# Optimization experiments

Measured on AMD Instinct MI355X. Metric: run time of the kernel, lower is better.

Reference implementation:

```python
import jax, jax.numpy as jnp
import numpy as np

B, N, T, E, R, NSEL = 128, 1000, 50, 32000, 4, 500
F0, CF = 3, 20
FS = 2 * CF + F0  # 43


def _conv(x, w, b):
    # NCHW valid conv, stride 1
    y = jax.lax.conv_general_dilated(x, w, (1, 1), 'VALID',
                                     dimension_numbers=('NCHW', 'OIHW', 'NCHW'))
    return y + b[None, :, None, None]


def setup_inputs() -> dict:
    key = jax.random.key(0)
    ks = jax.random.split(key, 20)
    s = 0.1
    return {
        'observation': jax.random.normal(ks[0], (B, F0, N, T), jnp.float32),
        'last_action': jax.random.uniform(ks[1], (B, NSEL + 1), jnp.float32),
        'w_s1': jax.random.normal(ks[2], (3, 3, 1, 3), jnp.float32) * s,
        'b_s1': jax.random.normal(ks[3], (3,), jnp.float32) * s,
        'w_s2': jax.random.normal(ks[4], (20, 3, 1, 48), jnp.float32) * s,
        'b_s2': jax.random.normal(ks[5], (20,), jnp.float32) * s,
        'w_m1': jax.random.normal(ks[6], (3, 3, 1, 21), jnp.float32) * s,
        'b_m1': jax.random.normal(ks[7], (3,), jnp.float32) * s,
        'w_m2': jax.random.normal(ks[8], (20, 3, 1, 30), jnp.float32) * s,
        'b_m2': jax.random.normal(ks[9], (20,), jnp.float32) * s,
        'w_rel': jax.random.normal(ks[10], (R, FS, FS), jnp.float32) * s,
        'w_root': jax.random.normal(ks[11], (FS, FS), jnp.float32) * s,
        'b_g': jax.random.normal(ks[12], (FS,), jnp.float32) * s,
        'w_fin': jax.random.normal(ks[13], (1, 2 * FS + 1, 1, 1), jnp.float32) * s,
        'b_fin': jax.random.normal(ks[14], (1,), jnp.float32) * s,
        'edge_index': jax.random.randint(ks[15], (2, E), 0, N, jnp.int64) if jax.config.jax_enable_x64 else jax.random.randint(ks[15], (2, E), 0, N).astype(jnp.int32),
        'edge_type': jax.random.randint(ks[16], (E,), 0, R).astype(jnp.int32),
        'nodes_to_select': jnp.sort(jax.random.randint(ks[17], (NSEL,), 0, N)).astype(jnp.int32),
    }


def reference(observation, last_action, w_s1, b_s1, w_s2, b_s2, w_m1, b_m1,
              w_m2, b_m2, w_rel, w_root, b_g, w_fin, b_fin,
              edge_index, edge_type, nodes_to_select):
    # temporal feature extraction
    short = jax.nn.relu(_conv(jax.nn.relu(_conv(observation, w_s1, b_s1)), w_s2, b_s2))
    mid = jax.nn.relu(_conv(jax.nn.relu(_conv(observation, w_m1, b_m1)), w_m2, b_m2))
    long = jax.nn.relu(jnp.max(observation, axis=3, keepdims=True))
    temporal = jnp.concatenate([short, mid, long], axis=1)  # [B, 43, N, 1]

    x = temporal[:, :, :, 0].transpose(0, 2, 1)  # [B, N, F]

    # RGCNConv with per-relation mean aggregation
    src, dst = edge_index[0], edge_index[1]
    xw = jnp.einsum('bnf,rfg->bnrg', x, w_rel)        # [B, N, R, F]
    msgs = xw[:, src, edge_type, :]                   # [B, E, F] gather
    seg = dst * R + edge_type                         # per (node, relation) segment
    agg = jax.vmap(lambda m: jax.ops.segment_sum(m, seg, num_segments=N * R))(msgs)
    cnt = jax.ops.segment_sum(jnp.ones((E,), x.dtype), seg, num_segments=N * R)
    inv = jnp.where(cnt > 0, 1.0 / cnt, 0.0)
    agg = (agg * inv[None, :, None]).reshape(B, N, R, FS).sum(axis=2)
    gout = jax.nn.leaky_relu(agg + x @ w_root + b_g, 0.01)  # [B, N, F]

    graph_features = gout.transpose(0, 2, 1)[..., None]     # [B, F, N, 1]
    feat = jnp.concatenate([temporal, graph_features], axis=1)  # [B, 86, N, 1]
    feat = feat[:, :, nodes_to_select, :]                       # [B, 86, NSEL, 1]
    last_stocks = last_action[:, 1:].reshape(B, 1, NSEL, 1)
    feat = jnp.concatenate([last_stocks, feat], axis=1)         # [B, 87, NSEL, 1]

    o = jnp.einsum('bcn,oc->bon', feat[..., 0], w_fin[:, :, 0, 0]) + b_fin[None, :, None]
    o = jnp.concatenate([jnp.zeros((B, 1, 1), o.dtype), o], axis=2)[:, 0, :]  # [B, NSEL+1]
    return jax.nn.softmax(o / 1.0, axis=-1)
```

## Files before the change

kernel.cpp:

```cpp
#include <hip/hip_runtime.h>
#include <math.h>

#define Bn 128
#define Nn 1000
#define Tn 50
#define En 32000
#define Rn 4
#define FSn 43
#define NSELn 500
#define NFtot (Nn * FSn)

__global__ __launch_bounds__(256, 4) void k_temporal(
    const float* __restrict__ obs,
    const float* __restrict__ w_s1, const float* __restrict__ b_s1,
    const float* __restrict__ w_s2, const float* __restrict__ b_s2,
    const float* __restrict__ w_m1, const float* __restrict__ b_m1,
    const float* __restrict__ w_m2, const float* __restrict__ b_m2,
    float* __restrict__ x)
{
    __shared__ float lds[3 * 64 * 51];

    const int b     = blockIdx.x;
    const int tile0 = blockIdx.y * 64;
    const int tid   = threadIdx.x;
    const int lane  = tid & 63;
    const int w     = __builtin_amdgcn_readfirstlane(tid >> 6);
    const int nrows = (Nn - tile0) < 64 ? (Nn - tile0) : 64;

    for (int c = 0; c < 3; ++c) {
        const float* srcp = obs + ((size_t)(b * 3 + c) * Nn + tile0) * Tn;
        for (int idx = tid; idx < nrows * Tn; idx += 256) {
            const int r = idx / Tn;
            const int t = idx - r * Tn;
            lds[(c * 64 + r) * 51 + t] = srcp[idx];
        }
    }
    __syncthreads();

    const int rb0 = (0 * 64 + lane) * 51;
    const int rb1 = (1 * 64 + lane) * 51;
    const int rb2 = (2 * 64 + lane) * 51;

    float acc[20];
    float mx0 = -1e30f, mx1 = -1e30f, mx2 = -1e30f;

    if (w < 2) {
        #pragma unroll
        for (int o = 0; o < 20; ++o) acc[o] = (w == 0) ? b_s2[o] : 0.f;

        const float s10 = b_s1[0], s11 = b_s1[1], s12 = b_s1[2];
        const int t0 = w * 24;

        #pragma unroll 1
        for (int t = t0; t < t0 + 24; ++t) {
            float v0 = s10, v1 = s11, v2 = s12;
            #pragma unroll
            for (int c = 0; c < 3; ++c) {
                const int base = (c * 64 + lane) * 51 + t;
                const float o0 = lds[base + 0];
                const float o1 = lds[base + 1];
                const float o2 = lds[base + 2];
                v0 += o0 * w_s1[(0 * 3 + c) * 3 + 0] + o1 * w_s1[(0 * 3 + c) * 3 + 1] + o2 * w_s1[(0 * 3 + c) * 3 + 2];
                v1 += o0 * w_s1[(1 * 3 + c) * 3 + 0] + o1 * w_s1[(1 * 3 + c) * 3 + 1] + o2 * w_s1[(1 * 3 + c) * 3 + 2];
                v2 += o0 * w_s1[(2 * 3 + c) * 3 + 0] + o1 * w_s1[(2 * 3 + c) * 3 + 1] + o2 * w_s1[(2 * 3 + c) * 3 + 2];
            }
            v0 = fmaxf(v0, 0.f); v1 = fmaxf(v1, 0.f); v2 = fmaxf(v2, 0.f);
            #pragma unroll
            for (int o = 0; o < 20; ++o) {
                acc[o] += v0 * w_s2[(o * 3 + 0) * 48 + t]
                        + v1 * w_s2[(o * 3 + 1) * 48 + t]
                        + v2 * w_s2[(o * 3 + 2) * 48 + t];
            }
        }

        const int l0 = w * 25;
        #pragma unroll 1
        for (int t = l0; t < l0 + 25; ++t) {
            mx0 = fmaxf(mx0, lds[rb0 + t]);
            mx1 = fmaxf(mx1, lds[rb1 + t]);
            mx2 = fmaxf(mx2, lds[rb2 + t]);
        }
    } else {
        #pragma unroll
        for (int o = 0; o < 20; ++o) acc[o] = (w == 2) ? b_m2[o] : 0.f;

        const float m10 = b_m1[0], m11 = b_m1[1], m12 = b_m1[2];
        const int t0 = (w - 2) * 15;

        #pragma unroll 1
        for (int t = t0; t < t0 + 15; ++t) {
            float u0 = m10, u1 = m11, u2 = m12;
            #pragma unroll
            for (int c = 0; c < 3; ++c) {
                const int base = (c * 64 + lane) * 51 + t;
                #pragma unroll
                for (int d = 0; d < 21; ++d) {
                    const float ov = lds[base + d];
                    u0 += ov * w_m1[(0 * 3 + c) * 21 + d];
                    u1 += ov * w_m1[(1 * 3 + c) * 21 + d];
                    u2 += ov * w_m1[(2 * 3 + c) * 21 + d];
                }
            }
            u0 = fmaxf(u0, 0.f); u1 = fmaxf(u1, 0.f); u2 = fmaxf(u2, 0.f);
            #pragma unroll
            for (int o = 0; o < 20; ++o) {
                acc[o] += u0 * w_m2[(o * 3 + 0) * 30 + t]
                        + u1 * w_m2[(o * 3 + 1) * 30 + t]
                        + u2 * w_m2[(o * 3 + 2) * 30 + t];
            }
        }
    }

    __syncthreads();
    float* pshort = lds;
    float* plong  = lds + 20 * 64;
    float* pmid   = lds + 23 * 64;

    if (w == 1) {
        #pragma unroll
        for (int o = 0; o < 20; ++o) pshort[o * 64 + lane] = acc[o];
        plong[0 * 64 + lane] = mx0;
        plong[1 * 64 + lane] = mx1;
        plong[2 * 64 + lane] = mx2;
    }
    if (w == 3) {
        #pragma unroll
        for (int o = 0; o < 20; ++o) pmid[o * 64 + lane] = acc[o];
    }
    __syncthreads();

    if (lane < nrows) {
        float* xp = x + ((size_t)b * Nn + tile0 + lane) * FSn;
        if (w == 0) {
            #pragma unroll
            for (int o = 0; o < 20; ++o)
                xp[o] = fmaxf(acc[o] + pshort[o * 64 + lane], 0.f);
            xp[40] = fmaxf(fmaxf(mx0, plong[0 * 64 + lane]), 0.f);
            xp[41] = fmaxf(fmaxf(mx1, plong[1 * 64 + lane]), 0.f);
            xp[42] = fmaxf(fmaxf(mx2, plong[2 * 64 + lane]), 0.f);
        } else if (w == 2) {
            #pragma unroll
            for (int o = 0; o < 20; ++o)
                xp[20 + o] = fmaxf(acc[o] + pmid[o * 64 + lane], 0.f);
        }
    }
}

__global__ __launch_bounds__(256) void k_transpose(const float* __restrict__ x,
                                                   float* __restrict__ xT)
{
    __shared__ float tile[64][129];
    const int c0  = blockIdx.x * 64;
    const int tid = threadIdx.x;

    const int j  = tid & 63;
    const int bs = tid >> 6;
    for (int bb = bs; bb < Bn; bb += 4) {
        int c = c0 + j;
        if (c < NFtot) tile[j][bb] = x[(size_t)bb * NFtot + c];
    }
    __syncthreads();

    const int b  = tid & 127;
    for (int jj = (tid >> 7); jj < 64; jj += 2) {
        int c = c0 + jj;
        if (c < NFtot) xT[(size_t)c * Bn + b] = tile[jj][b];
    }
}

__global__ void k_zero(int* __restrict__ cnt, int* __restrict__ pos)
{
    int i = blockIdx.x * blockDim.x + threadIdx.x;
    if (i < 4096) { cnt[i] = 0; pos[i] = 0; }
}

__global__ void k_count(const int* __restrict__ ei, const int* __restrict__ et,
                        int* __restrict__ cnt)
{
    int e = blockIdx.x * blockDim.x + threadIdx.x;
    if (e < En) {
        int dst = ei[En + e];
        atomicAdd(&cnt[dst * Rn + et[e]], 1);
    }
}

__global__ __launch_bounds__(1024) void k_scan(const int* __restrict__ cnt,
                                               int* __restrict__ off)
{
    __shared__ int sums[1024];
    int tid = threadIdx.x;
    int base = tid * 4;
    int c[4];
    int ts = 0;
    #pragma unroll
    for (int k = 0; k < 4; ++k) {
        int i = base + k;
        c[k] = (i < Nn * Rn) ? cnt[i] : 0;
        ts += c[k];
    }
    sums[tid] = ts;
    __syncthreads();
    for (int d = 1; d < 1024; d <<= 1) {
        int t = 0;
        if (tid >= d) t = sums[tid - d];
        __syncthreads();
        sums[tid] += t;
        __syncthreads();
    }
    int excl = sums[tid] - ts;
    #pragma unroll
    for (int k = 0; k < 4; ++k) {
        int i = base + k;
        off[i] = excl;
        excl += c[k];
    }
}

__global__ void k_fill(const int* __restrict__ ei, const int* __restrict__ et,
                       const int* __restrict__ off, int* __restrict__ pos,
                       int* __restrict__ csr)
{
    int e = blockIdx.x * blockDim.x + threadIdx.x;
    if (e < En) {
        int src = ei[e];
        int dst = ei[En + e];
        int seg = dst * Rn + et[e];
        int p = atomicAdd(&pos[seg], 1);
        csr[off[seg] + p] = src;
    }
}

__global__ __launch_bounds__(512) void k_gather(
    const float* __restrict__ xT,
    const float* __restrict__ w_rel, const float* __restrict__ w_root,
    const float* __restrict__ b_g,
    const float* __restrict__ w_fin, const float* __restrict__ b_fin,
    const float* __restrict__ la,
    const int* __restrict__ csr, const int* __restrict__ off,
    const int* __restrict__ cnt, const int* __restrict__ sel,
    float* __restrict__ logitT)
{
    __shared__ int   srcs[Rn][128];
    __shared__ int   scnt[Rn];
    __shared__ int   tcnt[Rn];
    __shared__ float red[FSn + 1][Bn];

    const int i   = blockIdx.x;
    const int dst = sel[i];
    const int tid = threadIdx.x;
    const int fs  = tid >> 7;
    const int b   = tid & 127;

    {
        const int r = fs;
        const int j = b;
        const int c = cnt[dst * Rn + r];
        const int o = off[dst * Rn + r];
        if (j == 0) { tcnt[r] = c; scnt[r] = (c < 128) ? c : 128; }
        if (j < c && j < 128) srcs[r][j] = csr[o + j];
    }
    __syncthreads();

    const int f0 = fs * 11;
    const int nf = (fs == 3) ? 10 : 11;

    float a[5][11];
    #pragma unroll
    for (int rr = 0; rr < 5; ++rr)
        #pragma unroll
        for (int k = 0; k < 11; ++k) a[rr][k] = 0.f;

    #pragma unroll
    for (int r = 0; r < Rn; ++r) {
        const int c = scnt[r];
        for (int j = 0; j < c; ++j) {
            const int src = srcs[r][j];
            const float* xp = xT + ((size_t)src * FSn + f0) * Bn + b;
            #pragma unroll
            for (int k = 0; k < 11; ++k)
                if (k < nf) a[r][k] += xp[(size_t)k * Bn];
        }
    }
    {
        const float* xp = xT + ((size_t)dst * FSn + f0) * Bn + b;
        #pragma unroll
        for (int k = 0; k < 11; ++k)
            if (k < nf) a[4][k] += xp[(size_t)k * Bn];
    }
    #pragma unroll
    for (int r = 0; r < Rn; ++r) {
        const int c = tcnt[r];
        const float iv = (c > 0) ? 1.f / (float)c : 0.f;
        #pragma unroll
        for (int k = 0; k < 11; ++k) a[r][k] *= iv;
    }

    float accg[FSn];
    #pragma unroll
    for (int g = 0; g < FSn; ++g) accg[g] = 0.f;
    float psum = 0.f;

    #pragma unroll
    for (int k = 0; k < 11; ++k) {
        if (k < nf) {
            const int f = f0 + k;
            #pragma unroll
            for (int rr = 0; rr < 5; ++rr) {
                const float av = a[rr][k];
                const float* wrow = (rr < 4)
                    ? (w_rel + ((size_t)rr * FSn + f) * FSn)
                    : (w_root + (size_t)f * FSn);
                #pragma unroll
                for (int g = 0; g < FSn; ++g) accg[g] += av * wrow[g];
            }
            psum += a[4][k] * w_fin[1 + f];
        }
    }

    if (fs == 3) {
        #pragma unroll
        for (int g = 0; g < FSn; ++g) red[g][b] = accg[g];
        red[FSn][b] = psum;
    }
    __syncthreads();
    if (fs == 2) {
        #pragma unroll
        for (int g = 0; g < FSn; ++g) red[g][b] += accg[g];
        red[FSn][b] += psum;
    }
    __syncthreads();
    if (fs == 1) {
        #pragma unroll
        for (int g = 0; g < FSn; ++g) red[g][b] += accg[g];
        red[FSn][b] += psum;
    }
    __syncthreads();
    if (fs == 0) {
        float logit = b_fin[0] + w_fin[0] * la[(size_t)b * (NSELn + 1) + 1 + i]
                    + psum + red[FSn][b];
        #pragma unroll
        for (int g = 0; g < FSn; ++g) {
            float v = accg[g] + red[g][b] + b_g[g];
            v = (v > 0.f) ? v : 0.01f * v;
            logit += v * w_fin[44 + g];
        }
        logitT[(size_t)i * Bn + b] = logit;
    }
}

__global__ __launch_bounds__(512) void k_softmax(const float* __restrict__ logitT,
                                                 float* __restrict__ out)
{
    __shared__ float red[512];
    const int b   = blockIdx.x;
    const int tid = threadIdx.x;

    const float l = (tid < NSELn) ? logitT[(size_t)tid * Bn + b] : -1e30f;
    red[tid] = l;
    __syncthreads();
    for (int s = 256; s > 0; s >>= 1) {
        if (tid < s) red[tid] = fmaxf(red[tid], red[tid + s]);
        __syncthreads();
    }
    const float m = fmaxf(red[0], 0.f);
    __syncthreads();

    const float e = (tid < NSELn) ? expf(l - m) : 0.f;
    red[tid] = e;
    __syncthreads();
    for (int s = 256; s > 0; s >>= 1) {
        if (tid < s) red[tid] += red[tid + s];
        __syncthreads();
    }
    const float e0  = expf(-m);
    const float inv = 1.f / (red[0] + e0);

    if (tid == 0) out[(size_t)b * (NSELn + 1)] = e0 * inv;
    if (tid < NSELn) out[(size_t)b * (NSELn + 1) + 1 + tid] = e * inv;
}

extern "C" void kernel_launch(void* const* d_in, const int* in_sizes, int n_in,
                              void* d_out, int out_size, void* d_ws, size_t ws_size,
                              hipStream_t stream)
{
    const float* obs    = (const float*)d_in[0];
    const float* la     = (const float*)d_in[1];
    const float* w_s1   = (const float*)d_in[2];
    const float* b_s1   = (const float*)d_in[3];
    const float* w_s2   = (const float*)d_in[4];
    const float* b_s2   = (const float*)d_in[5];
    const float* w_m1   = (const float*)d_in[6];
    const float* b_m1   = (const float*)d_in[7];
    const float* w_m2   = (const float*)d_in[8];
    const float* b_m2   = (const float*)d_in[9];
    const float* w_rel  = (const float*)d_in[10];
    const float* w_root = (const float*)d_in[11];
    const float* b_g    = (const float*)d_in[12];
    const float* w_fin  = (const float*)d_in[13];
    const float* b_fin  = (const float*)d_in[14];
    const int*   ei     = (const int*)d_in[15];
    const int*   et     = (const int*)d_in[16];
    const int*   sel    = (const int*)d_in[17];
    float*       out    = (float*)d_out;

    float* x      = (float*)d_ws;
    float* xT     = x + 5504000;
    int*   cnt    = (int*)(xT + 5504000);
    int*   offb   = cnt + 4096;
    int*   pos    = offb + 4096;
    int*   csr    = pos + 4096;
    float* logitT = x;

    hipLaunchKernelGGL(k_zero,  dim3(16),  dim3(256), 0, stream, cnt, pos);
    hipLaunchKernelGGL(k_count, dim3((En + 255) / 256), dim3(256), 0, stream, ei, et, cnt);
    hipLaunchKernelGGL(k_scan,  dim3(1),   dim3(1024), 0, stream, cnt, offb);
    hipLaunchKernelGGL(k_fill,  dim3((En + 255) / 256), dim3(256), 0, stream, ei, et, offb, pos, csr);

    hipLaunchKernelGGL(k_temporal, dim3(Bn, (Nn + 63) / 64), dim3(256), 0, stream,
                       obs, w_s1, b_s1, w_s2, b_s2, w_m1, b_m1, w_m2, b_m2, x);

    hipLaunchKernelGGL(k_transpose, dim3((NFtot + 63) / 64), dim3(256), 0, stream, x, xT);

    hipLaunchKernelGGL(k_gather, dim3(NSELn), dim3(512), 0, stream,
                       xT, w_rel, w_root, b_g, w_fin, b_fin, la,
                       csr, offb, cnt, sel, logitT);

    hipLaunchKernelGGL(k_softmax, dim3(Bn), dim3(512), 0, stream, logitT, out);
}
```

Measured before the change: 258.4 us.

## Split graph gather into per-relation aggregation kernel and restructure temporal convolutions

The fused gather-plus-transform kernel is split in two. A new kernel runs one block per (selected node, relation) and does a float4 vectorised neighbour sum into a workspace buffer. A second kernel reads these means and applies the relation and root weights. This gives four times more blocks for the memory-bound gather, at the cost of an extra global round trip. The temporal kernel is also changed: the short conv gets a sliding-window register reuse, and the mid conv is rewritten as a fully unrolled scatter over input positions so each LDS value is read once instead of 21 times. This raises register pressure, and the workspace layout is reorganised so the larger abar buffer fits.

```diff
diff --git a/kernel.cpp b/kernel.cpp
--- a/kernel.cpp
+++ b/kernel.cpp
@@ -10,6 +10,48 @@
 #define NSELn 500
 #define NFtot (Nn * FSn)
 
+template<int T0>
+__device__ __forceinline__ void mid_part(const float* __restrict__ lds, int lane,
+    const float* __restrict__ w_m1, const float* __restrict__ w_m2,
+    float bm0, float bm1v, float bm2, float* __restrict__ acc)
+{
+    float y0[15], y1[15], y2[15];
+    #pragma unroll
+    for (int t = 0; t < 15; ++t) { y0[t] = bm0; y1[t] = bm1v; y2[t] = bm2; }
+
+    const int rb0 = (0 * 64 + lane) * 51;
+    const int rb1 = (1 * 64 + lane) * 51;
+    const int rb2 = (2 * 64 + lane) * 51;
+
+    #pragma unroll
+    for (int tau = T0; tau < T0 + 35; ++tau) {
+        const int tlo = (tau - 20 > T0) ? (tau - 20) : T0;
+        const int thi = (tau < T0 + 14) ? tau : (T0 + 14);
+        const float o0 = lds[rb0 + tau];
+        const float o1 = lds[rb1 + tau];
+        const float o2 = lds[rb2 + tau];
+        #pragma unroll
+        for (int t = tlo; t <= thi; ++t) {
+            const int d = tau - t;
+            y0[t - T0] += o0 * w_m1[  0 + d] + o1 * w_m1[ 21 + d] + o2 * w_m1[ 42 + d];
+            y1[t - T0] += o0 * w_m1[ 63 + d] + o1 * w_m1[ 84 + d] + o2 * w_m1[105 + d];
+            y2[t - T0] += o0 * w_m1[126 + d] + o1 * w_m1[147 + d] + o2 * w_m1[168 + d];
+        }
+    }
+    #pragma unroll
+    for (int tt = 0; tt < 15; ++tt) {
+        const float u0 = fmaxf(y0[tt], 0.f);
+        const float u1 = fmaxf(y1[tt], 0.f);
+        const float u2 = fmaxf(y2[tt], 0.f);
+        #pragma unroll
+        for (int o = 0; o < 20; ++o) {
+            acc[o] += u0 * w_m2[(o * 3 + 0) * 30 + T0 + tt]
+                    + u1 * w_m2[(o * 3 + 1) * 30 + T0 + tt]
+                    + u2 * w_m2[(o * 3 + 2) * 30 + T0 + tt];
+        }
+    }
+}
+
 __global__ __launch_bounds__(256, 4) void k_temporal(
     const float* __restrict__ obs,
     const float* __restrict__ w_s1, const float* __restrict__ b_s1,
@@ -37,10 +79,6 @@
     }
     __syncthreads();
 
-    const int rb0 = (0 * 64 + lane) * 51;
-    const int rb1 = (1 * 64 + lane) * 51;
-    const int rb2 = (2 * 64 + lane) * 51;
-
     float acc[20];
     float mx0 = -1e30f, mx1 = -1e30f, mx2 = -1e30f;
 
@@ -50,31 +88,44 @@
 
         const float s10 = b_s1[0], s11 = b_s1[1], s12 = b_s1[2];
         const int t0 = w * 24;
-
-        #pragma unroll 1
-        for (int t = t0; t < t0 + 24; ++t) {
-            float v0 = s10, v1 = s11, v2 = s12;
-            #pragma unroll
-            for (int c = 0; c < 3; ++c) {
-                const int base = (c * 64 + lane) * 51 + t;
-                const float o0 = lds[base + 0];
-                const float o1 = lds[base + 1];
-                const float o2 = lds[base + 2];
-                v0 += o0 * w_s1[(0 * 3 + c) * 3 + 0] + o1 * w_s1[(0 * 3 + c) * 3 + 1] + o2 * w_s1[(0 * 3 + c) * 3 + 2];
-                v1 += o0 * w_s1[(1 * 3 + c) * 3 + 0] + o1 * w_s1[(1 * 3 + c) * 3 + 1] + o2 * w_s1[(1 * 3 + c) * 3 + 2];
-                v2 += o0 * w_s1[(2 * 3 + c) * 3 + 0] + o1 * w_s1[(2 * 3 + c) * 3 + 1] + o2 * w_s1[(2 * 3 + c) * 3 + 2];
-            }
+        const int base0 = (0 * 64 + lane) * 51 + t0;
+        const int base1 = (1 * 64 + lane) * 51 + t0;
+        const int base2 = (2 * 64 + lane) * 51 + t0;
+
+        float a0 = lds[base0], p0 = lds[base0 + 1];
+        float a1 = lds[base1], p1 = lds[base1 + 1];
+        float a2 = lds[base2], p2 = lds[base2 + 1];
+
+        #pragma unroll 3
+        for (int t = 0; t < 24; ++t) {
+            const float c0 = lds[base0 + t + 2];
+            const float c1 = lds[base1 + t + 2];
+            const float c2 = lds[base2 + t + 2];
+            float v0 = s10 + a0 * w_s1[0]  + p0 * w_s1[1]  + c0 * w_s1[2]
+                           + a1 * w_s1[3]  + p1 * w_s1[4]  + c1 * w_s1[5]
+                           + a2 * w_s1[6]  + p2 * w_s1[7]  + c2 * w_s1[8];
+            float v1 = s11 + a0 * w_s1[9]  + p0 * w_s1[10] + c0 * w_s1[11]
+                           + a1 * w_s1[12] + p1 * w_s1[13] + c1 * w_s1[14]
+                           + a2 * w_s1[15] + p2 * w_s1[16] + c2 * w_s1[17];
+            float v2 = s12 + a0 * w_s1[18] + p0 * w_s1[19] + c0 * w_s1[20]
+                           + a1 * w_s1[21] + p1 * w_s1[22] + c1 * w_s1[23]
+                           + a2 * w_s1[24] + p2 * w_s1[25] + c2 * w_s1[26];
             v0 = fmaxf(v0, 0.f); v1 = fmaxf(v1, 0.f); v2 = fmaxf(v2, 0.f);
+            const int tt = t0 + t;
             #pragma unroll
             for (int o = 0; o < 20; ++o) {
-                acc[o] += v0 * w_s2[(o * 3 + 0) * 48 + t]
-                        + v1 * w_s2[(o * 3 + 1) * 48 + t]
-                        + v2 * w_s2[(o * 3 + 2) * 48 + t];
+                acc[o] += v0 * w_s2[(o * 3 + 0) * 48 + tt]
+                        + v1 * w_s2[(o * 3 + 1) * 48 + tt]
+                        + v2 * w_s2[(o * 3 + 2) * 48 + tt];
             }
-        }
-
+            a0 = p0; p0 = c0; a1 = p1; p1 = c1; a2 = p2; p2 = c2;
+        }
+
+        const int rb0 = (0 * 64 + lane) * 51;
+        const int rb1 = (1 * 64 + lane) * 51;
+        const int rb2 = (2 * 64 + lane) * 51;
         const int l0 = w * 25;
-        #pragma unroll 1
+        #pragma unroll 5
         for (int t = l0; t < l0 + 25; ++t) {
             mx0 = fmaxf(mx0, lds[rb0 + t]);
             mx1 = fmaxf(mx1, lds[rb1 + t]);
@@ -83,32 +134,9 @@
     } else {
         #pragma unroll
         for (int o = 0; o < 20; ++o) acc[o] = (w == 2) ? b_m2[o] : 0.f;
-
         const float m10 = b_m1[0], m11 = b_m1[1], m12 = b_m1[2];
-        const int t0 = (w - 2) * 15;
-
-        #pragma unroll 1
-        for (int t = t0; t < t0 + 15; ++t) {
-            float u0 = m10, u1 = m11, u2 = m12;
-            #pragma unroll
-            for (int c = 0; c < 3; ++c) {
-                const int base = (c * 64 + lane) * 51 + t;
-                #pragma unroll
-                for (int d = 0; d < 21; ++d) {
-                    const float ov = lds[base + d];
-                    u0 += ov * w_m1[(0 * 3 + c) * 21 + d];
-                    u1 += ov * w_m1[(1 * 3 + c) * 21 + d];
-                    u2 += ov * w_m1[(2 * 3 + c) * 21 + d];
-                }
-            }
-            u0 = fmaxf(u0, 0.f); u1 = fmaxf(u1, 0.f); u2 = fmaxf(u2, 0.f);
-            #pragma unroll
-            for (int o = 0; o < 20; ++o) {
-                acc[o] += u0 * w_m2[(o * 3 + 0) * 30 + t]
-                        + u1 * w_m2[(o * 3 + 1) * 30 + t]
-                        + u2 * w_m2[(o * 3 + 2) * 30 + t];
-            }
-        }
+        if (w == 2) mid_part<0 >(lds, lane, w_m1, w_m2, m10, m11, m12, acc);
+        else        mid_part<15>(lds, lane, w_m1, w_m2, m10, m11, m12, acc);
     }
 
     __syncthreads();
@@ -230,19 +258,69 @@
     }
 }
 
-__global__ __launch_bounds__(512) void k_gather(
+__global__ __launch_bounds__(256) void k_agg4(
     const float* __restrict__ xT,
+    const int* __restrict__ csr, const int* __restrict__ off,
+    const int* __restrict__ cnt, const int* __restrict__ sel,
+    float* __restrict__ abar)
+{
+    __shared__ int srcs[128];
+
+    const int blk = blockIdx.x;
+    const int i   = blk >> 2;
+    const int r   = blk & 3;
+    const int dst = sel[i];
+    const int tid = threadIdx.x;
+    const int b4  = tid & 31;
+    const int fc  = tid >> 5;
+
+    const int seg = dst * Rn + r;
+    const int c   = cnt[seg];
+    const int o   = off[seg];
+    const int cc  = (c < 128) ? c : 128;
+    if (tid < cc) srcs[tid] = csr[o + tid];
+    __syncthreads();
+
+    const int nk = (fc < 3) ? 6 : 5;
+
+    float4 acc[6];
+    #pragma unroll
+    for (int k = 0; k < 6; ++k) acc[k] = make_float4(0.f, 0.f, 0.f, 0.f);
+
+    const float4* xT4 = (const float4*)xT;
+    for (int j = 0; j < cc; ++j) {
+        const int src = srcs[j];
+        const float4* base = xT4 + (size_t)src * (FSn * 32) + (size_t)fc * 32 + b4;
+        #pragma unroll
+        for (int k = 0; k < 6; ++k) {
+            if (k < nk) {
+                const float4 v = base[k * 8 * 32];
+                acc[k].x += v.x; acc[k].y += v.y; acc[k].z += v.z; acc[k].w += v.w;
+            }
+        }
+    }
+
+    const float inv = (c > 0) ? 1.f / (float)c : 0.f;
+    float4* ab4 = (float4*)abar + (size_t)(i * Rn + r) * (FSn * 32) + (size_t)fc * 32 + b4;
+    #pragma unroll
+    for (int k = 0; k < 6; ++k) {
+        if (k < nk) {
+            float4 v = acc[k];
+            v.x *= inv; v.y *= inv; v.z *= inv; v.w *= inv;
+            ab4[k * 8 * 32] = v;
+        }
+    }
+}
+
+__global__ __launch_bounds__(512) void k_trans(
+    const float* __restrict__ xT, const float* __restrict__ abar,
     const float* __restrict__ w_rel, const float* __restrict__ w_root,
     const float* __restrict__ b_g,
     const float* __restrict__ w_fin, const float* __restrict__ b_fin,
     const float* __restrict__ la,
-    const int* __restrict__ csr, const int* __restrict__ off,
-    const int* __restrict__ cnt, const int* __restrict__ sel,
+    const int* __restrict__ sel,
     float* __restrict__ logitT)
 {
-    __shared__ int   srcs[Rn][128];
-    __shared__ int   scnt[Rn];
-    __shared__ int   tcnt[Rn];
     __shared__ float red[FSn + 1][Bn];
 
     const int i   = blockIdx.x;
@@ -251,48 +329,22 @@
     const int fs  = tid >> 7;
     const int b   = tid & 127;
 
-    {
-        const int r = fs;
-        const int j = b;
-        const int c = cnt[dst * Rn + r];
-        const int o = off[dst * Rn + r];
-        if (j == 0) { tcnt[r] = c; scnt[r] = (c < 128) ? c : 128; }
-        if (j < c && j < 128) srcs[r][j] = csr[o + j];
-    }
-    __syncthreads();
-
     const int f0 = fs * 11;
     const int nf = (fs == 3) ? 10 : 11;
 
     float a[5][11];
     #pragma unroll
-    for (int rr = 0; rr < 5; ++rr)
-        #pragma unroll
-        for (int k = 0; k < 11; ++k) a[rr][k] = 0.f;
-
-    #pragma unroll
-    for (int r = 0; r < Rn; ++r) {
-        const int c = scnt[r];
-        for (int j = 0; j < c; ++j) {
-            const int src = srcs[r][j];
-            const float* xp = xT + ((size_t)src * FSn + f0) * Bn + b;
-            #pragma unroll
-            for (int k = 0; k < 11; ++k)
-                if (k < nf) a[r][k] += xp[(size_t)k * Bn];
-        }
+    for (int rr = 0; rr < 4; ++rr) {
+        const float* ap = abar + ((size_t)(i * Rn + rr) * FSn + f0) * Bn + b;
+        #pragma unroll
+        for (int k = 0; k < 11; ++k)
+            a[rr][k] = (k < nf) ? ap[(size_t)k * Bn] : 0.f;
     }
     {
         const float* xp = xT + ((size_t)dst * FSn + f0) * Bn + b;
         #pragma unroll
         for (int k = 0; k < 11; ++k)
-            if (k < nf) a[4][k] += xp[(size_t)k * Bn];
-    }
-    #pragma unroll
-    for (int r = 0; r < Rn; ++r) {
-        const int c = tcnt[r];
-        const float iv = (c > 0) ? 1.f / (float)c : 0.f;
-        #pragma unroll
-        for (int k = 0; k < 11; ++k) a[r][k] *= iv;
+            a[4][k] = (k < nf) ? xp[(size_t)k * Bn] : 0.f;
     }
 
     float accg[FSn];
@@ -403,13 +455,14 @@
     const int*   sel    = (const int*)d_in[17];
     float*       out    = (float*)d_out;
 
-    float* x      = (float*)d_ws;
-    float* xT     = x + 5504000;
+    float* abar   = (float*)d_ws;
+    float* x      = abar;
+    float* xT     = abar + 11008000;
     int*   cnt    = (int*)(xT + 5504000);
     int*   offb   = cnt + 4096;
     int*   pos    = offb + 4096;
     int*   csr    = pos + 4096;
-    float* logitT = x;
+    float* logitT = (float*)(csr + 32000);
 
     hipLaunchKernelGGL(k_zero,  dim3(16),  dim3(256), 0, stream, cnt, pos);
     hipLaunchKernelGGL(k_count, dim3((En + 255) / 256), dim3(256), 0, stream, ei, et, cnt);
@@ -421,9 +474,11 @@
 
     hipLaunchKernelGGL(k_transpose, dim3((NFtot + 63) / 64), dim3(256), 0, stream, x, xT);
 
-    hipLaunchKernelGGL(k_gather, dim3(NSELn), dim3(512), 0, stream,
-                       xT, w_rel, w_root, b_g, w_fin, b_fin, la,
-                       csr, offb, cnt, sel, logitT);
+    hipLaunchKernelGGL(k_agg4, dim3(NSELn * Rn), dim3(256), 0, stream,
+                       xT, csr, offb, cnt, sel, abar);
+
+    hipLaunchKernelGGL(k_trans, dim3(NSELn), dim3(512), 0, stream,
+                       xT, abar, w_rel, w_root, b_g, w_fin, b_fin, la, sel, logitT);
 
     hipLaunchKernelGGL(k_softmax, dim3(Bn), dim3(512), 0, stream, logitT, out);
 }
```

New measurement: 501.7 us. 1.94x slower.
